# Optimization experiments

Measured on AMD Instinct MI355X. Metric: run time of the kernel, lower is better.

The kernel has to match this reference:

```python
import jax, jax.numpy as jnp
import numpy as np

BUFFER_C = 1.25

def setup_inputs() -> dict:
    key = jax.random.key(0)
    k1, k2, k3 = jax.random.split(key, 3)
    T, D, E = 4096, 1024, 8
    x = jax.random.normal(k1, (T, D), dtype=jnp.float32)
    Wg = jax.random.normal(k2, (D, E), dtype=jnp.float32) / np.sqrt(D)
    bg = jnp.zeros((E,), dtype=jnp.float32)
    W = jax.random.normal(k3, (E, D, D), dtype=jnp.float32) / np.sqrt(D)
    b = jnp.zeros((E, D), dtype=jnp.float32)
    return {"x": x, "Wg": Wg, "bg": bg, "W": W, "b": b}


def reference(x, Wg, bg, W, b):
    # Top-1 (Switch-style) routing with capacity buffer, per-expert Linear,
    # prob-weighted combine, plus load-balancing aux loss.
    T, D = x.shape
    E = W.shape[0]
    capacity = int(BUFFER_C * T / E)

    logits = x @ Wg + bg                      # [T, E]
    probs = jax.nn.softmax(logits, axis=-1)   # [T, E]
    top_idx = jnp.argmax(probs, axis=-1)      # [T]
    top_prob = jnp.take_along_axis(probs, top_idx[:, None], axis=-1)[:, 0]

    onehot = jax.nn.one_hot(top_idx, E, dtype=x.dtype)       # [T, E]
    # 1-indexed position of each token within its expert's buffer
    pos = jnp.cumsum(onehot, axis=0) * onehot                # [T, E]
    dispatch = jnp.where((onehot > 0) & (pos <= capacity), 1.0, 0.0).astype(x.dtype)

    # dense dispatch/combine equivalent of the masked per-expert loop
    xe = jnp.einsum('te,td->etd', dispatch, x)               # [E, T, D]
    ye = jnp.einsum('etd,edf->etf', xe, W) + b[:, None, :]   # [E, T, D]
    y = jnp.einsum('te,etf->tf', dispatch, ye)               # [T, D] (0 for dropped)
    out = y * top_prob[:, None]

    # aux load-balance loss: E * sum_e f_e * P_e
    f = onehot.mean(axis=0)
    P = probs.mean(axis=0)
    aux_loss = E * jnp.sum(f * P)
    return out, aux_loss
```

## Files before the change

kernel.cpp:

```cpp
#include <hip/hip_runtime.h>
#include <hip/hip_bf16.h>
#include <cstdint>

#define T_TOK 4096
#define D_DIM 1024
#define E_EXP 8
#define CAP   640
#define MAXDROP 3456
#define MT    10
#define GBLK  1024

typedef __attribute__((ext_vector_type(8))) short short8;
typedef __attribute__((ext_vector_type(4))) float f32x4;

__device__ inline unsigned short f2bf(float f) {
    uint32_t u = __float_as_uint(f);
    u += 0x7fffu + ((u >> 16) & 1u);
    return (unsigned short)(u >> 16);
}

__device__ inline void dma16(const void* g, void* l) {
    __builtin_amdgcn_global_load_lds(
        (const __attribute__((address_space(1))) unsigned int*)g,
        (__attribute__((address_space(3))) unsigned int*)l, 16, 0, 0);
}

#define WB_TILE(e, nt, kt) ((((size_t)(e) * 16 + (nt)) * 16 + (kt)) * 4096)
#define XG_TILE(e, mt, kt) ((((size_t)(e) * MT + (mt)) * 16 + (kt)) * 4096)

__global__ __launch_bounds__(256) void prep_kernel(
    const float* __restrict__ x, const float* __restrict__ Wg,
    const float* __restrict__ bg, const float* __restrict__ W,
    unsigned short* __restrict__ Wb,
    int* __restrict__ top_idx, float* __restrict__ top_prob,
    float* __restrict__ blkpart)
{
    int bid = blockIdx.x;
    int tid = threadIdx.x;

    if (bid >= GBLK) {
        int bid2 = (bid - GBLK) * 2;
        int e   = bid2 >> 8;
        int kt  = (bid2 >> 4) & 15;
        int ntA = bid2 & 15;
        int k0  = kt * 64;
        const float* Wsrc = W + (size_t)e * D_DIM * D_DIM + (size_t)k0 * D_DIM;

        int c0 = tid, c1 = tid + 256;
        int g0 = c0 >> 6, n0c = c0 & 63;
        int g1 = c1 >> 6, n1c = c1 & 63;

        #pragma unroll
        for (int half = 0; half < 2; half++) {
            int n0 = (ntA + half) * 64;
            unsigned short* dst = Wb + WB_TILE(e, ntA + half, kt);
            const float* s0 = Wsrc + (size_t)(g0 * 8) * D_DIM + n0 + n0c;
            const float* s1 = Wsrc + (size_t)(g1 * 8) * D_DIM + n0 + n1c;
            float v[8], u[8];
            #pragma unroll
            for (int z = 0; z < 8; z++) v[z] = s0[(size_t)z * D_DIM];
            #pragma unroll
            for (int z = 0; z < 8; z++) u[z] = s1[(size_t)z * D_DIM];
            short8 a, b2;
            #pragma unroll
            for (int z = 0; z < 8; z++) { a[z] = (short)f2bf(v[z]); b2[z] = (short)f2bf(u[z]); }
            *(short8*)&dst[(size_t)c0 * 8] = a;
            *(short8*)&dst[(size_t)c1 * 8] = b2;
        }
    } else {
        __shared__ float probs_sm[4][8];
        int wid  = tid >> 6;
        int lane = tid & 63;
        int t = bid * 4 + wid;

        const float* xr = x + (size_t)t * D_DIM;

        float acc[8];
        #pragma unroll
        for (int e = 0; e < 8; e++) acc[e] = 0.f;

        #pragma unroll
        for (int ii = 0; ii < 16; ii++) {
            int d = lane + 64 * ii;
            float xv = xr[d];
            const float4* wr = (const float4*)(Wg + (size_t)d * 8);
            float4 a = wr[0], bq = wr[1];
            acc[0] += xv * a.x;  acc[1] += xv * a.y;
            acc[2] += xv * a.z;  acc[3] += xv * a.w;
            acc[4] += xv * bq.x; acc[5] += xv * bq.y;
            acc[6] += xv * bq.z; acc[7] += xv * bq.w;
        }
        #pragma unroll
        for (int off = 32; off > 0; off >>= 1) {
            #pragma unroll
            for (int e = 0; e < 8; e++) acc[e] += __shfl_xor(acc[e], off, 64);
        }
        if (lane == 0) {
            float lg[8];
            #pragma unroll
            for (int e = 0; e < 8; e++) lg[e] = acc[e] + bg[e];
            float m = lg[0]; int am = 0;
            #pragma unroll
            for (int e = 1; e < 8; e++) { if (lg[e] > m) { m = lg[e]; am = e; } }
            float ex[8], s = 0.f;
            #pragma unroll
            for (int e = 0; e < 8; e++) { ex[e] = __expf(lg[e] - m); s += ex[e]; }
            float inv = 1.f / s;
            top_idx[t]  = am;
            top_prob[t] = ex[am] * inv;
            #pragma unroll
            for (int e = 0; e < 8; e++) probs_sm[wid][e] = ex[e] * inv;
        }
        __syncthreads();
        if (tid < 8) {
            float s = probs_sm[0][tid] + probs_sm[1][tid]
                    + probs_sm[2][tid] + probs_sm[3][tid];
            blkpart[(size_t)bid * 8 + tid] = s;
        }
    }
}

__global__ __launch_bounds__(1024) void scan_kernel(
    const int* __restrict__ top_idx,
    int* __restrict__ tok_list, int* __restrict__ cnt,
    const float* __restrict__ blkpart,
    float* __restrict__ out, float* __restrict__ out_aux)
{
    __shared__ int counts[64][8];
    __shared__ int excl[64][8];
    __shared__ int fulltot[8];
    __shared__ int droplist[MAXDROP];
    __shared__ int ndrop;
    __shared__ float wpart[16][8];

    int tid  = threadIdx.x;
    int wv   = tid >> 6;
    int lane = tid & 63;
    unsigned long long ltmask = (lane == 0) ? 0ull : ((~0ull) >> (64 - lane));

    if (tid == 0) ndrop = 0;

    float p[8];
    {
        const float4* bp = (const float4*)(blkpart + (size_t)tid * 8);
        float4 p0 = bp[0], p1 = bp[1];
        p[0] = p0.x; p[1] = p0.y; p[2] = p0.z; p[3] = p0.w;
        p[4] = p1.x; p[5] = p1.y; p[6] = p1.z; p[7] = p1.w;
    }

    int ecache[4];
    #pragma unroll
    for (int c = 0; c < 4; c++)
        ecache[c] = top_idx[(4 * wv + c) * 64 + lane];

    #pragma unroll
    for (int c = 0; c < 4; c++) {
        int chunk = 4 * wv + c;
        int e = ecache[c];
        #pragma unroll
        for (int q = 0; q < 8; q++) {
            unsigned long long mk = __ballot(e == q);
            int tot = __popcll(mk);
            if (lane == q) counts[chunk][q] = tot;
        }
    }
    __syncthreads();

    if (wv == 0) {
        #pragma unroll
        for (int q = 0; q < 8; q++) {
            int v = counts[lane][q];
            int orig = v;
            #pragma unroll
            for (int off = 1; off < 64; off <<= 1) {
                int n = __shfl_up(v, off, 64);
                if (lane >= off) v += n;
            }
            excl[lane][q] = v - orig;
            int total = __shfl(v, 63, 64);
            if (lane == 0) {
                fulltot[q] = total;
                cnt[q] = total < CAP ? total : CAP;
            }
        }
    }
    __syncthreads();

    #pragma unroll
    for (int c = 0; c < 4; c++) {
        int chunk = 4 * wv + c;
        int t = chunk * 64 + lane;
        int e = ecache[c];
        int pos = 0;
        #pragma unroll
        for (int q = 0; q < 8; q++) {
            unsigned long long mk = __ballot(e == q);
            if (e == q) pos = excl[chunk][q] + __popcll(mk & ltmask);
        }
        if (pos < CAP) {
            tok_list[e * CAP + pos] = t;
        } else {
            int di = atomicAdd(&ndrop, 1);
            droplist[di] = t;
        }
    }

    #pragma unroll
    for (int off = 32; off > 0; off >>= 1) {
        #pragma unroll
        for (int e = 0; e < 8; e++) p[e] += __shfl_xor(p[e], off, 64);
    }
    if (lane == 0) {
        #pragma unroll
        for (int e = 0; e < 8; e++) wpart[wv][e] = p[e];
    }
    __syncthreads();

    int nd = ndrop;
    int grp = tid >> 8;
    int col = (tid & 255) * 4;
    float4 z = {0.f, 0.f, 0.f, 0.f};
    for (int d = grp; d < nd; d += 4) {
        int row = droplist[d];
        *(float4*)&out[(size_t)row * D_DIM + col] = z;
    }

    if (tid == 0) {
        float s = 0.f;
        #pragma unroll
        for (int e = 0; e < 8; e++) {
            float Pe = 0.f;
            #pragma unroll
            for (int w = 0; w < 16; w++) Pe += wpart[w][e];
            s += ((float)fulltot[e] / (float)T_TOK) * (Pe / (float)T_TOK);
        }
        out_aux[0] = (float)E_EXP * s;
    }
}

__global__ __launch_bounds__(256) void gather_kernel(
    const float* __restrict__ x, const int* __restrict__ tok_list,
    const int* __restrict__ cnt, unsigned short* __restrict__ xg)
{
    int bid = blockIdx.x;
    int e   = bid / (MT * 16);
    int rem = bid % (MT * 16);
    int mt  = rem >> 4, kt = rem & 15;
    int count = cnt[e];
    int m0 = mt * 64;
    if (m0 >= count) return;

    int tid = threadIdx.x;
    const int* tl = tok_list + e * CAP;
    unsigned short* dst = xg + XG_TILE(e, mt, kt);

    #pragma unroll
    for (int p = 0; p < 2; p++) {
        int c = tid + 256 * p;
        int g = c >> 6, row = c & 63;
        int gm = m0 + row;
        int tok = tl[gm < count ? gm : count - 1];
        const float* src = x + (size_t)tok * D_DIM + kt * 64 + g * 8;
        float4 v0 = *(const float4*)(src);
        float4 v1 = *(const float4*)(src + 4);
        short8 v;
        v[0] = f2bf(v0.x); v[1] = f2bf(v0.y); v[2] = f2bf(v0.z); v[3] = f2bf(v0.w);
        v[4] = f2bf(v1.x); v[5] = f2bf(v1.y); v[6] = f2bf(v1.z); v[7] = f2bf(v1.w);
        *(short8*)&dst[(size_t)c * 8] = v;
    }
}

__device__ inline void stage_dma(const unsigned short* gAt, const unsigned short* gBt,
                                 unsigned short (*Ab)[64][8], unsigned short (*Bb)[64][8],
                                 int w, int lane)
{
    size_t lo = (size_t)lane * 8;
    dma16(gAt + (size_t)w * 512 + lo,       &Ab[w][0][0]);
    dma16(gAt + (size_t)(w + 4) * 512 + lo, &Ab[w + 4][0][0]);
    dma16(gBt + (size_t)w * 512 + lo,       &Bb[w][0][0]);
    dma16(gBt + (size_t)(w + 4) * 512 + lo, &Bb[w + 4][0][0]);
}

__global__ __launch_bounds__(256) void expert_gemm(
    const unsigned short* __restrict__ xg, const unsigned short* __restrict__ Wb,
    const float* __restrict__ bias,
    const int* __restrict__ tok_list, const int* __restrict__ cnt,
    const float* __restrict__ top_prob, float* __restrict__ out)
{
    int bid = blockIdx.x;
    int e   = bid / (MT * 16);
    int rem = bid % (MT * 16);
    int mt  = rem >> 4, nt = rem & 15;
    int count = cnt[e];
    int m0 = mt * 64;
    if (m0 >= count) return;
    int n0 = nt * 64;

    __shared__ unsigned short Ab[2][8][64][8];
    __shared__ unsigned short Bb[2][8][64][8];

    int tid  = threadIdx.x;
    int lane = tid & 63, w = tid >> 6;
    int quad = lane >> 4, l16 = lane & 15;
    int mw = (w >> 1) * 32, nw = (w & 1) * 32;

    const int* tl = tok_list + e * CAP;
    const unsigned short* gA0 = xg + XG_TILE(e, mt, 0);
    const unsigned short* gB0 = Wb + WB_TILE(e, nt, 0);

    f32x4 acc[2][2];
    #pragma unroll
    for (int i = 0; i < 2; i++)
        #pragma unroll
        for (int j = 0; j < 2; j++)
            acc[i][j] = (f32x4){0.f, 0.f, 0.f, 0.f};

    stage_dma(gA0, gB0, Ab[0], Bb[0], w, lane);

    int cur = 0;
    #pragma unroll 1
    for (int kt = 0; kt < 16; kt++) {
        __syncthreads();
        if (kt + 1 < 16)
            stage_dma(gA0 + (size_t)(kt + 1) * 4096, gB0 + (size_t)(kt + 1) * 4096,
                      Ab[cur ^ 1], Bb[cur ^ 1], w, lane);

        short8 af[2][2], bf[2][2];
        #pragma unroll
        for (int s = 0; s < 2; s++) {
            #pragma unroll
            for (int i = 0; i < 2; i++) {
                af[s][i] = *(const short8*)&Ab[cur][s * 4 + quad][mw + 16 * i + l16][0];
                bf[s][i] = *(const short8*)&Bb[cur][s * 4 + quad][nw + 16 * i + l16][0];
            }
        }
        #pragma unroll
        for (int s = 0; s < 2; s++)
            #pragma unroll
            for (int i = 0; i < 2; i++)
                #pragma unroll
                for (int j = 0; j < 2; j++)
                    acc[i][j] = __builtin_amdgcn_mfma_f32_16x16x32_bf16(
                        af[s][i], bf[s][j], acc[i][j], 0, 0, 0);
        cur ^= 1;
    }

    float bv[2];
    #pragma unroll
    for (int j = 0; j < 2; j++)
        bv[j] = bias[e * D_DIM + n0 + nw + 16 * j + l16];

    #pragma unroll
    for (int i = 0; i < 2; i++) {
        int rb = m0 + mw + 16 * i + quad * 4;
        #pragma unroll
        for (int r = 0; r < 4; r++) {
            int gm = rb + r;
            if (gm >= count) continue;
            int tok = tl[gm];
            float p = top_prob[tok];
            float* orow = out + (size_t)tok * D_DIM + n0 + nw + l16;
            #pragma unroll
            for (int j = 0; j < 2; j++)
                orow[16 * j] = (acc[i][j][r] + bv[j]) * p;
        }
    }
}

extern "C" void kernel_launch(void* const* d_in, const int* in_sizes, int n_in,
                              void* d_out, int out_size, void* d_ws, size_t ws_size,
                              hipStream_t stream) {
    const float* x  = (const float*)d_in[0];
    const float* Wg = (const float*)d_in[1];
    const float* bg = (const float*)d_in[2];
    const float* W  = (const float*)d_in[3];
    const float* b  = (const float*)d_in[4];
    float* out = (float*)d_out;

    char* ws = (char*)d_ws;
    unsigned short* Wb = (unsigned short*)(ws + 0);
    unsigned short* xg = (unsigned short*)(ws + 16777216);
    int*   top_idx  = (int*)(ws + 27262976);
    float* top_prob = (float*)(ws + 27279360);
    int*   tok_list = (int*)(ws + 27295744);
    int*   cnt      = (int*)(ws + 27316224);
    float* blkpart  = (float*)(ws + 27316256);

    hipLaunchKernelGGL(prep_kernel, dim3(GBLK + 1024), dim3(256), 0, stream,
                       x, Wg, bg, W, Wb, top_idx, top_prob, blkpart);
    hipLaunchKernelGGL(scan_kernel, dim3(1), dim3(1024), 0, stream,
                       top_idx, tok_list, cnt, blkpart, out, out + (size_t)T_TOK * D_DIM);
    hipLaunchKernelGGL(gather_kernel, dim3(E_EXP * MT * 16), dim3(256), 0, stream,
                       x, tok_list, cnt, xg);
    hipLaunchKernelGGL(expert_gemm, dim3(E_EXP * MT * 16), dim3(256), 0, stream,
                       xg, Wb, b, tok_list, cnt, top_prob, out);
}
```

Baseline: 142.6 us.

## Enlarge expert GEMM tiles to 128x128 with 512 threads and triple-buffered DMA

The expert GEMM now uses 128x128 output tiles per block with 8 waves, each wave computing a 64x32 sub-tile. K is split into 32 half-tiles that are fed through a three-stage LDS ring using async global-to-LDS loads, explicit vmcnt waits and raw barriers. The goal is more reuse of each loaded A and B tile and better hiding of load latency. The cost is fewer blocks (320 instead of 1280), which lowers parallelism on a GPU with many CUs, and wasted work on partially filled M tiles.

```diff
diff --git a/kernel.cpp b/kernel.cpp
--- a/kernel.cpp
+++ b/kernel.cpp
@@ -9,6 +9,7 @@
 #define MAXDROP 3456
 #define MT    10
 #define GBLK  1024
+#define NSUB  32
 
 typedef __attribute__((ext_vector_type(8))) short short8;
 typedef __attribute__((ext_vector_type(4))) float f32x4;
@@ -270,96 +271,103 @@
     }
 }
 
-__device__ inline void stage_dma(const unsigned short* gAt, const unsigned short* gBt,
-                                 unsigned short (*Ab)[64][8], unsigned short (*Bb)[64][8],
-                                 int w, int lane)
-{
-    size_t lo = (size_t)lane * 8;
-    dma16(gAt + (size_t)w * 512 + lo,       &Ab[w][0][0]);
-    dma16(gAt + (size_t)(w + 4) * 512 + lo, &Ab[w + 4][0][0]);
-    dma16(gBt + (size_t)w * 512 + lo,       &Bb[w][0][0]);
-    dma16(gBt + (size_t)(w + 4) * 512 + lo, &Bb[w + 4][0][0]);
-}
-
-__global__ __launch_bounds__(256) void expert_gemm(
+__global__ __launch_bounds__(512) void expert_gemm(
     const unsigned short* __restrict__ xg, const unsigned short* __restrict__ Wb,
     const float* __restrict__ bias,
     const int* __restrict__ tok_list, const int* __restrict__ cnt,
     const float* __restrict__ top_prob, float* __restrict__ out)
 {
     int bid = blockIdx.x;
-    int e   = bid / (MT * 16);
-    int rem = bid % (MT * 16);
-    int mt  = rem >> 4, nt = rem & 15;
+    int e   = bid / 40;
+    int rem = bid % 40;
+    int mtb = rem >> 3, ntb = rem & 7;
     int count = cnt[e];
-    int m0 = mt * 64;
+    int m0 = mtb * 128;
     if (m0 >= count) return;
-    int n0 = nt * 64;
-
-    __shared__ unsigned short Ab[2][8][64][8];
-    __shared__ unsigned short Bb[2][8][64][8];
+    int n0 = ntb * 128;
+
+    __shared__ unsigned short Ab[3][2][4][64][8];
+    __shared__ unsigned short Bb[3][2][4][64][8];
 
     int tid  = threadIdx.x;
     int lane = tid & 63, w = tid >> 6;
     int quad = lane >> 4, l16 = lane & 15;
-    int mw = (w >> 1) * 32, nw = (w & 1) * 32;
+    int wr = w >> 2, wc = w & 3;
 
     const int* tl = tok_list + e * CAP;
-    const unsigned short* gA0 = xg + XG_TILE(e, mt, 0);
-    const unsigned short* gB0 = Wb + WB_TILE(e, nt, 0);
-
-    f32x4 acc[2][2];
-    #pragma unroll
-    for (int i = 0; i < 2; i++)
+
+    int  wa    = w & 3;
+    int  shalf = wa >> 1;
+    int  sg0   = (wa & 1) * 2;
+    const unsigned short* sbase =
+        (w < 4) ? (xg + XG_TILE(e, 2 * mtb + shalf, 0) + (size_t)lane * 8)
+                : (Wb + WB_TILE(e, 2 * ntb + shalf, 0) + (size_t)lane * 8);
+
+    #define STAGE(s, buf) do {                                                  \
+        size_t off_ = (size_t)((s) >> 1) * 4096 + (size_t)((s) & 1) * 2048;     \
+        if (w < 4) {                                                            \
+            dma16(sbase + off_ + (size_t)sg0 * 512,       &Ab[buf][shalf][sg0][0][0]);     \
+            dma16(sbase + off_ + (size_t)(sg0 + 1) * 512, &Ab[buf][shalf][sg0 + 1][0][0]); \
+        } else {                                                                \
+            dma16(sbase + off_ + (size_t)sg0 * 512,       &Bb[buf][shalf][sg0][0][0]);     \
+            dma16(sbase + off_ + (size_t)(sg0 + 1) * 512, &Bb[buf][shalf][sg0 + 1][0][0]); \
+        }                                                                       \
+    } while (0)
+
+    f32x4 acc[4][2];
+    #pragma unroll
+    for (int i = 0; i < 4; i++)
         #pragma unroll
         for (int j = 0; j < 2; j++)
             acc[i][j] = (f32x4){0.f, 0.f, 0.f, 0.f};
 
-    stage_dma(gA0, gB0, Ab[0], Bb[0], w, lane);
-
-    int cur = 0;
+    STAGE(0, 0);
+    STAGE(1, 1);
+
     #pragma unroll 1
-    for (int kt = 0; kt < 16; kt++) {
-        __syncthreads();
-        if (kt + 1 < 16)
-            stage_dma(gA0 + (size_t)(kt + 1) * 4096, gB0 + (size_t)(kt + 1) * 4096,
-                      Ab[cur ^ 1], Bb[cur ^ 1], w, lane);
-
-        short8 af[2][2], bf[2][2];
-        #pragma unroll
-        for (int s = 0; s < 2; s++) {
-            #pragma unroll
-            for (int i = 0; i < 2; i++) {
-                af[s][i] = *(const short8*)&Ab[cur][s * 4 + quad][mw + 16 * i + l16][0];
-                bf[s][i] = *(const short8*)&Bb[cur][s * 4 + quad][nw + 16 * i + l16][0];
-            }
-        }
-        #pragma unroll
-        for (int s = 0; s < 2; s++)
-            #pragma unroll
-            for (int i = 0; i < 2; i++)
-                #pragma unroll
-                for (int j = 0; j < 2; j++)
-                    acc[i][j] = __builtin_amdgcn_mfma_f32_16x16x32_bf16(
-                        af[s][i], bf[s][j], acc[i][j], 0, 0, 0);
-        cur ^= 1;
-    }
+    for (int s = 0; s < NSUB; s++) {
+        if (s + 1 < NSUB) { asm volatile("s_waitcnt vmcnt(2)" ::: "memory"); }
+        else              { asm volatile("s_waitcnt vmcnt(0)" ::: "memory"); }
+        __builtin_amdgcn_s_barrier();
+        __builtin_amdgcn_sched_barrier(0);
+
+        int cur = s % 3;
+        if (s + 2 < NSUB)
+            STAGE(s + 2, (s + 2) % 3);
+
+        short8 af[4], bf[2];
+        #pragma unroll
+        for (int i = 0; i < 4; i++)
+            af[i] = *(const short8*)&Ab[cur][wr][quad][16 * i + l16][0];
+        #pragma unroll
+        for (int j = 0; j < 2; j++) {
+            int cb = wc * 32 + 16 * j;
+            bf[j] = *(const short8*)&Bb[cur][cb >> 6][quad][(cb & 63) + l16][0];
+        }
+        #pragma unroll
+        for (int i = 0; i < 4; i++)
+            #pragma unroll
+            for (int j = 0; j < 2; j++)
+                acc[i][j] = __builtin_amdgcn_mfma_f32_16x16x32_bf16(
+                    af[i], bf[j], acc[i][j], 0, 0, 0);
+    }
+    #undef STAGE
 
     float bv[2];
     #pragma unroll
     for (int j = 0; j < 2; j++)
-        bv[j] = bias[e * D_DIM + n0 + nw + 16 * j + l16];
-
-    #pragma unroll
-    for (int i = 0; i < 2; i++) {
-        int rb = m0 + mw + 16 * i + quad * 4;
+        bv[j] = bias[e * D_DIM + n0 + wc * 32 + 16 * j + l16];
+
+    #pragma unroll
+    for (int i = 0; i < 4; i++) {
+        int rb = m0 + wr * 64 + 16 * i + quad * 4;
         #pragma unroll
         for (int r = 0; r < 4; r++) {
             int gm = rb + r;
             if (gm >= count) continue;
             int tok = tl[gm];
             float p = top_prob[tok];
-            float* orow = out + (size_t)tok * D_DIM + n0 + nw + l16;
+            float* orow = out + (size_t)tok * D_DIM + n0 + wc * 32 + l16;
             #pragma unroll
             for (int j = 0; j < 2; j++)
                 orow[16 * j] = (acc[i][j][r] + bv[j]) * p;
@@ -392,6 +400,6 @@
                        top_idx, tok_list, cnt, blkpart, out, out + (size_t)T_TOK * D_DIM);
     hipLaunchKernelGGL(gather_kernel, dim3(E_EXP * MT * 16), dim3(256), 0, stream,
                        x, tok_list, cnt, xg);
-    hipLaunchKernelGGL(expert_gemm, dim3(E_EXP * MT * 16), dim3(256), 0, stream,
+    hipLaunchKernelGGL(expert_gemm, dim3(E_EXP * 5 * 8), dim3(512), 0, stream,
                        xg, Wb, b, tok_list, cnt, top_prob, out);
 }
```

Result: no change. 139.9 us (-1.9%).
